# Performance work log

Measured on AMD Instinct MI355X. Metric: run time of the kernel, lower is better.

Reference implementation:

```python
import jax, jax.numpy as jnp
import numpy as np

N_POI, EMBED, N_EDGES, N_LAYERS, N_HEADS = 50000, 128, 800000, 2, 4
B, L = 512, 64  # sessions, session length (equal-length sections)


def setup_inputs() -> dict:
    key = jax.random.key(0)
    ks = jax.random.split(key, 12)
    d = EMBED
    return {
        "poi_embeds": jax.random.normal(ks[0], (N_POI, d), jnp.float32),
        "dist_edges": jax.random.randint(ks[1], (2, N_EDGES), 0, N_POI),
        "dist_vec": jax.random.uniform(ks[2], (N_EDGES,), jnp.float32),
        "data_poi": jax.random.randint(ks[3], (B,), 0, N_POI),
        "data_x": jax.random.randint(ks[4], (B * L,), 0, N_POI),
        "lin_w": jax.random.normal(ks[5], (N_LAYERS, d, d), jnp.float32) / np.sqrt(d),
        "lin_b": jnp.zeros((N_LAYERS, d), jnp.float32),
        "in_proj_w": jax.random.normal(ks[6], (3 * d, d), jnp.float32) / np.sqrt(d),
        "in_proj_b": jnp.zeros((3 * d,), jnp.float32),
        "out_proj_w": jax.random.normal(ks[7], (d, d), jnp.float32) / np.sqrt(d),
        "out_proj_b": jnp.zeros((d,), jnp.float32),
    }


def reference(poi_embeds, dist_edges, dist_vec, data_poi, data_x,
              lin_w, lin_b, in_proj_w, in_proj_b, out_proj_w, out_proj_b):
    n_poi, d = poi_embeds.shape
    # --- edge augmentation done in GeoGraph.__init__: reversed edges + self loops ---
    loop = jnp.arange(n_poi)
    edges = jnp.concatenate([dist_edges, dist_edges[::-1], jnp.stack([loop, loop])], axis=1)
    dvec = jnp.concatenate([dist_vec, dist_vec, jnp.zeros((n_poi,), dist_vec.dtype)])
    src, dst = edges[0], edges[1]
    # degree of source nodes (torch_geometric.utils.degree on nodes1)
    deg = jnp.zeros((n_poi,), poi_embeds.dtype).at[src].add(1.0)
    w = jax.lax.rsqrt(deg[src] * deg[dst]) * jnp.exp(-dvec ** 2)  # [E]

    enc = poi_embeds
    for i in range(lin_w.shape[0]):
        h = enc @ lin_w[i].T + lin_b[i]                              # [N, d]
        msg = w[:, None] * h[dst]                                    # [E, d] gather
        agg = jax.ops.segment_sum(msg, src, num_segments=n_poi)      # [N, d] scatter
        agg = jnp.where(agg >= 0, agg, 0.01 * agg)                   # leaky_relu(0.01)
        enc = agg / jnp.maximum(jnp.linalg.norm(agg, axis=-1, keepdims=True), 1e-12)

    tar_embed = enc[data_poi]                                        # [B, d]
    seq = enc[data_x].reshape(B, L, d)                               # padded sessions

    # --- nn.MultiheadAttention (batch_first) ---
    hd = d // N_HEADS
    qkv = seq @ in_proj_w.T + in_proj_b                              # [B, L, 3d]
    q, k, v = jnp.split(qkv, 3, axis=-1)
    heads = lambda t: t.reshape(B, L, N_HEADS, hd).transpose(0, 2, 1, 3)
    q, k, v = heads(q), heads(k), heads(v)
    scores = jnp.einsum('bhqd,bhkd->bhqk', q, k) / np.sqrt(hd)
    attn = jax.nn.softmax(scores, axis=-1)
    o = jnp.einsum('bhqk,bhkd->bhqd', attn, v).transpose(0, 2, 1, 3).reshape(B, L, d)
    o = o @ out_proj_w.T + out_proj_b

    aggr_feat = o.mean(axis=1)                                       # mean over padded length
    return aggr_feat, tar_embed
```

## Files before the change

### kernel.cpp

```cpp
#include <hip/hip_runtime.h>
#include <hip/hip_fp16.h>

#define NPOI 50000
#define EMB 128
#define NEDGE 800000
#define EAUG (2 * NEDGE + NPOI)
#define BATCH 512
#define SEQL 64
#define NHEADS 4
#define HDIM 32
#define NB 196
#define P1_BLOCKS ((NEDGE + 2047) / 2048)
#define SLAB_CAP 10240
#define BUCKET_CAP 10240

typedef _Float16 half8 __attribute__((ext_vector_type(8)));
typedef _Float16 half4 __attribute__((ext_vector_type(4)));
typedef _Float16 half2t __attribute__((ext_vector_type(2)));
typedef float f32x4 __attribute__((ext_vector_type(4)));
typedef unsigned long long u64;

union HBits { _Float16 h; unsigned short u; };


#define N4_POI (NPOI * 128 / 4)
#define N4_LIN (2 * 128 * 128 / 4)
#define N4_INW (384 * 128 / 4)
#define CVT_TOT (N4_POI + N4_LIN + N4_INW + NB)

__global__ void cvt_all_kernel(const float* __restrict__ poi, const float* __restrict__ linw,
                               const float* __restrict__ inw,
                               _Float16* __restrict__ poi_h, _Float16* __restrict__ linw_h,
                               _Float16* __restrict__ inw_h, int* __restrict__ bcur) {
    int i = blockIdx.x * blockDim.x + threadIdx.x;
    const float* src; _Float16* dst; int j = i;
    if (i < N4_POI) { src = poi; dst = poi_h; }
    else if (i < N4_POI + N4_LIN) { j = i - N4_POI; src = linw; dst = linw_h; }
    else if (i < N4_POI + N4_LIN + N4_INW) { j = i - N4_POI - N4_LIN; src = inw; dst = inw_h; }
    else if (i < CVT_TOT) { int b = i - (N4_POI + N4_LIN + N4_INW); bcur[b] = b * SLAB_CAP; return; }
    else return;
    float4 v = ((const float4*)src)[j];
    half4 h = { (_Float16)v.x, (_Float16)v.y, (_Float16)v.z, (_Float16)v.w };
    ((half4*)dst)[j] = h;
}


__global__ __launch_bounds__(256) void partition_kernel(
    const int* __restrict__ e0, const int* __restrict__ e1,
    const float* __restrict__ dv, int* __restrict__ bcur,
    u64* __restrict__ staging)
{
    __shared__ u64 stg[4096];
    __shared__ int lh[NB], lbase[NB], gb[NB];
    __shared__ int sc[256];
    const int t = threadIdx.x;
    const int blockBase = blockIdx.x * 2048;
    for (int j = t; j < NB; j += 256) lh[j] = 0;
    __syncthreads();

    u64 vals[16];
    unsigned br[16];
#pragma unroll
    for (int i = 0; i < 8; ++i) {
        br[2 * i] = 0xFFFFFFFFu;
        br[2 * i + 1] = 0xFFFFFFFFu;
        int g = blockBase + i * 256 + t;
        if (g < NEDGE) {
            int s = e0[g], d = e1[g];
            unsigned db = __float_as_uint(dv[g]);
            vals[2 * i]     = ((u64)s << 48) | ((u64)d << 32) | db;
            vals[2 * i + 1] = ((u64)d << 48) | ((u64)s << 32) | db;
            int bs = s >> 8, bd = d >> 8;
            int rs = atomicAdd(&lh[bs], 1);
            int rd_ = atomicAdd(&lh[bd], 1);
            br[2 * i]     = ((unsigned)bs << 16) | (unsigned)rs;
            br[2 * i + 1] = ((unsigned)bd << 16) | (unsigned)rd_;
        }
    }
    __syncthreads();
    sc[t] = (t < NB) ? lh[t] : 0;
    __syncthreads();
    for (int o = 1; o < 256; o <<= 1) {
        int u = (t >= o) ? sc[t - o] : 0;
        __syncthreads();
        sc[t] += u;
        __syncthreads();
    }
    if (t < NB) {
        lbase[t] = sc[t] - lh[t];
        gb[t] = (lh[t] > 0) ? atomicAdd(&bcur[t], lh[t]) : 0;
    }
    __syncthreads();
#pragma unroll
    for (int i = 0; i < 16; ++i) {
        if (br[i] != 0xFFFFFFFFu) {
            int b = br[i] >> 16, r = br[i] & 0xFFFF;
            stg[lbase[b] + r] = vals[i];
        }
    }
    __syncthreads();
    const int total = sc[255];
    for (int j = t; j < total; j += 256) {
        u64 v = stg[j];
        int b = (int)(v >> 56);
        staging[(size_t)gb[b] + (unsigned)(j - lbase[b])] = v;
    }
}


__global__ __launch_bounds__(256) void csr_sort_kernel(
    const u64* __restrict__ staging, const int* __restrict__ bcur,
    float* __restrict__ rd, int* __restrict__ offs, unsigned* __restrict__ ew)
{
    const int k = blockIdx.x;
    const int node0 = k * 256;
    __shared__ unsigned outb[BUCKET_CAP];
    __shared__ int cnt[256], base2[256];
    __shared__ float rdl[256];
    __shared__ int bb_sh;
    const int t = threadIdx.x;
    const int node = node0 + t;
    {
        int partial = 0;
        for (int j = t; j < k; j += 256) partial += (bcur[j] - j * SLAB_CAP) + 256;
        base2[t] = partial;
        __syncthreads();
        for (int o = 128; o > 0; o >>= 1) {
            if (t < o) base2[t] += base2[t + o];
            __syncthreads();
        }
        if (t == 0) bb_sh = base2[0];
        __syncthreads();
    }
    const int bucketbase = bb_sh;
    __syncthreads();
    cnt[t] = 0;
    __syncthreads();
    const int sb = k * SLAB_CAP;
    const int n = bcur[k] - sb;
    for (int j = t; j < n; j += 256)
        atomicAdd(&cnt[(int)(staging[sb + j] >> 48) & 255], 1);
    __syncthreads();
    int rowsz = (node < NPOI) ? cnt[t] + 1 : 0;
    if (node < NPOI) {
        float r_ = rsqrtf((float)rowsz);
        rd[node] = r_;
        rdl[t] = r_;
    } else rdl[t] = 0.f;
    base2[t] = rowsz;
    __syncthreads();
    for (int o = 1; o < 256; o <<= 1) {
        int u = (t >= o) ? base2[t - o] : 0;
        __syncthreads();
        base2[t] += u;
        __syncthreads();
    }
    int myexc = base2[t] - rowsz;
    __syncthreads();
    base2[t] = myexc;
    cnt[t] = 0;
    if (node < NPOI) {
        offs[node] = bucketbase + myexc;
        if (node == NPOI - 1) offs[NPOI] = bucketbase + myexc + rowsz;
    }
    __syncthreads();
    for (int j = t; j < n; j += 256) {
        u64 e = staging[sb + j];
        int sl = (int)(e >> 48) & 255;
        int d = (int)(e >> 32) & 0xFFFF;
        float dist = __uint_as_float((unsigned)e);
        float w = rdl[sl] * expf(-dist * dist);
        HBits cv; cv.h = (_Float16)w;
        int r = atomicAdd(&cnt[sl], 1);
        outb[base2[sl] + r] = ((unsigned)d << 16) | cv.u;
    }
    __syncthreads();
    if (node < NPOI) {
        HBits cv; cv.h = (_Float16)rdl[t];
        outb[base2[t] + cnt[t]] = ((unsigned)node << 16) | cv.u;
    }
    __syncthreads();
    const int ntot = n + ((node0 + 256 <= NPOI) ? 256 : (NPOI - node0));
    for (int j = t; j < ntot; j += 256) ew[bucketbase + j] = outb[j];
}


__global__ __launch_bounds__(256) void gemm_mfma_f16(
    const _Float16* __restrict__ A, const int* __restrict__ gidx,
    const _Float16* __restrict__ B, const float* __restrict__ bias,
    const float* __restrict__ rs,
    _Float16* __restrict__ C, int M, int N)
{
    __shared__ _Float16 Asl[64][136];
    __shared__ _Float16 Bsl[64][136];
    const int tid = threadIdx.x;
    const int n0 = blockIdx.x * 64;
    const int m0 = blockIdx.y * 64;

#pragma unroll
    for (int i = 0; i < 4; ++i) {
        int u = i * 256 + tid;
        int r = u >> 4;
        int c = u & 15;
        int row = m0 + r;
        int ar = (row < M) ? (gidx ? gidx[row] : row) : 0;
        *(float4*)&Asl[r][c * 8] = *(const float4*)(A + (size_t)ar * 128 + c * 8);
        *(float4*)&Bsl[r][c * 8] = *(const float4*)(B + (size_t)(n0 + r) * 128 + c * 8);
    }
    __syncthreads();

    const int wave = tid >> 6;
    const int lane = tid & 63;
    const int l15 = lane & 15;
    const int quad = lane >> 4;

    f32x4 acc[4];
#pragma unroll
    for (int mt = 0; mt < 4; ++mt) acc[mt] = (f32x4){0.f, 0.f, 0.f, 0.f};

#pragma unroll
    for (int ks = 0; ks < 4; ++ks) {
        half8 bfrag = *(const half8*)&Bsl[wave * 16 + l15][quad * 8 + ks * 32];
#pragma unroll
        for (int mt = 0; mt < 4; ++mt) {
            half8 afrag = *(const half8*)&Asl[mt * 16 + l15][quad * 8 + ks * 32];
            acc[mt] = __builtin_amdgcn_mfma_f32_16x16x32_f16(afrag, bfrag, acc[mt], 0, 0, 0);
        }
    }

    const int col = wave * 16 + l15;
    const float bv = bias[n0 + col];
    __syncthreads();
#pragma unroll
    for (int mt = 0; mt < 4; ++mt)
#pragma unroll
        for (int r = 0; r < 4; ++r) {
            int m = m0 + mt * 16 + quad * 4 + r;
            float v = acc[mt][r] + bv;
            if (rs) { int mm = (m < M) ? m : 0; v *= rs[mm]; }
            Asl[mt * 16 + quad * 4 + r][col] = (_Float16)v;
        }
    __syncthreads();
#pragma unroll
    for (int i = 0; i < 2; ++i) {
        int u = i * 256 + tid;
        int r = u >> 3;
        int c = u & 7;
        int m = m0 + r;
        if (m < M)
            *(half8*)(C + (size_t)m * N + n0 + c * 8) = *(const half8*)&Asl[r][c * 8];
    }
}


__global__ __launch_bounds__(64) void aggregate_kernel(
    const _Float16* __restrict__ h, const int* __restrict__ offs,
    const unsigned* __restrict__ ew, _Float16* __restrict__ enc_h)
{
    const int row = blockIdx.x;
    const int lane = threadIdx.x;
    const int beg = offs[row];
    const int end = offs[row + 1];
    float ax = 0.f, ay = 0.f;
#pragma unroll 8
    for (int e = beg; e < end; ++e) {
        unsigned p = ew[e];
        HBits cv; cv.u = (unsigned short)(p & 0xffffu);
        float w = (float)cv.h;
        int d = p >> 16;
        half2t hv = *(const half2t*)(h + (size_t)d * 128 + lane * 2);
        ax += w * (float)hv[0];
        ay += w * (float)hv[1];
    }
    ax = ax >= 0.f ? ax : 0.01f * ax;
    ay = ay >= 0.f ? ay : 0.01f * ay;
    float ss = ax * ax + ay * ay;
#pragma unroll
    for (int o = 32; o > 0; o >>= 1) ss += __shfl_xor(ss, o);
    float inv = 1.f / fmaxf(sqrtf(ss), 1e-12f);
    half2t hv = { (_Float16)(ax * inv), (_Float16)(ay * inv) };
    *(half2t*)(enc_h + (size_t)row * 128 + lane * 2) = hv;
}


__global__ __launch_bounds__(256) void attn_mfma_kernel(
    const _Float16* __restrict__ qkv, const float* __restrict__ outw,
    const float* __restrict__ outb, const _Float16* __restrict__ enc_h,
    const int* __restrict__ data_poi, float* __restrict__ out)
{
    const int b = blockIdx.x;
    const int wave = threadIdx.x >> 6;
    const int lane = threadIdx.x & 63;
    const int l15 = lane & 15;
    const int quad = lane >> 4;
    __shared__ _Float16 pP[NHEADS][64][72];
    __shared__ _Float16 vT[NHEADS][32][72];
    __shared__ float ob[128];
    const _Float16* base = qkv + (size_t)b * SEQL * 384;

    {
        const _Float16* vrow = base + (size_t)lane * 384 + 256 + wave * 32;
        half8 v0 = *(const half8*)(vrow);
        half8 v1 = *(const half8*)(vrow + 8);
        half8 v2 = *(const half8*)(vrow + 16);
        half8 v3 = *(const half8*)(vrow + 24);
#pragma unroll
        for (int j = 0; j < 8; ++j) {
            vT[wave][j][lane]      = v0[j];
            vT[wave][j + 8][lane]  = v1[j];
            vT[wave][j + 16][lane] = v2[j];
            vT[wave][j + 24][lane] = v3[j];
        }
    }

    half8 qf[4], kf[4];
#pragma unroll
    for (int t = 0; t < 4; ++t) {
        qf[t] = *(const half8*)(base + (size_t)(t * 16 + l15) * 384 + wave * 32 + quad * 8);
        kf[t] = *(const half8*)(base + (size_t)(t * 16 + l15) * 384 + 128 + wave * 32 + quad * 8);
    }

    f32x4 S[4][4];
#pragma unroll
    for (int lt = 0; lt < 4; ++lt)
#pragma unroll
        for (int mt = 0; mt < 4; ++mt) S[lt][mt] = (f32x4){0.f, 0.f, 0.f, 0.f};
#pragma unroll
    for (int lt = 0; lt < 4; ++lt)
#pragma unroll
        for (int mt = 0; mt < 4; ++mt)
            S[lt][mt] = __builtin_amdgcn_mfma_f32_16x16x32_f16(qf[lt], kf[mt], S[lt][mt], 0, 0, 0);

    const float scale = 0.17677669529663687f;
#pragma unroll
    for (int lt = 0; lt < 4; ++lt) {
#pragma unroll
        for (int r = 0; r < 4; ++r) {
            float m0 = -1e30f;
#pragma unroll
            for (int mt = 0; mt < 4; ++mt) {
                S[lt][mt][r] *= scale;
                m0 = fmaxf(m0, S[lt][mt][r]);
            }
#pragma unroll
            for (int o = 1; o < 16; o <<= 1) m0 = fmaxf(m0, __shfl_xor(m0, o));
            float s0 = 0.f;
#pragma unroll
            for (int mt = 0; mt < 4; ++mt) {
                float p = __expf(S[lt][mt][r] - m0);
                S[lt][mt][r] = p;
                s0 += p;
            }
#pragma unroll
            for (int o = 1; o < 16; o <<= 1) s0 += __shfl_xor(s0, o);
            float inv = 1.f / s0;
#pragma unroll
            for (int mt = 0; mt < 4; ++mt)
                pP[wave][lt * 16 + quad * 4 + r][mt * 16 + l15] = (_Float16)(S[lt][mt][r] * inv);
        }
    }
    __syncthreads();

    f32x4 O[4][2];
#pragma unroll
    for (int lt = 0; lt < 4; ++lt)
#pragma unroll
        for (int jt = 0; jt < 2; ++jt) O[lt][jt] = (f32x4){0.f, 0.f, 0.f, 0.f};
#pragma unroll
    for (int kh = 0; kh < 2; ++kh) {
        half8 vf[2];
#pragma unroll
        for (int jt = 0; jt < 2; ++jt)
            vf[jt] = *(const half8*)&vT[wave][jt * 16 + l15][kh * 32 + quad * 8];
#pragma unroll
        for (int lt = 0; lt < 4; ++lt) {
            half8 pf = *(const half8*)&pP[wave][lt * 16 + l15][kh * 32 + quad * 8];
#pragma unroll
            for (int jt = 0; jt < 2; ++jt)
                O[lt][jt] = __builtin_amdgcn_mfma_f32_16x16x32_f16(pf, vf[jt], O[lt][jt], 0, 0, 0);
        }
    }

#pragma unroll
    for (int jt = 0; jt < 2; ++jt) {
        float part = 0.f;
#pragma unroll
        for (int lt = 0; lt < 4; ++lt)
#pragma unroll
            for (int r = 0; r < 4; ++r) part += O[lt][jt][r];
        part += __shfl_xor(part, 16);
        part += __shfl_xor(part, 32);
        if (quad == 0) ob[wave * 32 + jt * 16 + l15] = part * (1.f / 64.f);
    }
    __syncthreads();

    int t = threadIdx.x;
    if (t < 128) {
        float val = outb[t];
        const float* wrow = outw + (size_t)t * 128;
#pragma unroll 8
        for (int k4 = 0; k4 < 32; ++k4) {
            float4 wv = *(const float4*)(wrow + k4 * 4);
            val += wv.x * ob[k4 * 4] + wv.y * ob[k4 * 4 + 1]
                 + wv.z * ob[k4 * 4 + 2] + wv.w * ob[k4 * 4 + 3];
        }
        out[(size_t)b * 128 + t] = val;
    } else {
        int j = t - 128;
        out[(size_t)(BATCH + b) * 128 + j] = (float)enc_h[(size_t)data_poi[b] * 128 + j];
    }
}


extern "C" void kernel_launch(void* const* d_in, const int* in_sizes, int n_in,
                              void* d_out, int out_size, void* d_ws, size_t ws_size,
                              hipStream_t stream)
{
    const float* poi      = (const float*)d_in[0];
    const int*   edges    = (const int*)d_in[1];
    const float* dvec     = (const float*)d_in[2];
    const int*   data_poi = (const int*)d_in[3];
    const int*   data_x   = (const int*)d_in[4];
    const float* lin_w    = (const float*)d_in[5];
    const float* lin_b    = (const float*)d_in[6];
    const float* inw      = (const float*)d_in[7];
    const float* inb      = (const float*)d_in[8];
    const float* outw     = (const float*)d_in[9];
    const float* outb     = (const float*)d_in[10];
    const int* e0 = edges;
    const int* e1 = edges + NEDGE;

    char* ws = (char*)d_ws;
    size_t off = 0;
    auto alloc = [&](size_t bytes) -> void* {
        void* p = ws + off;
        off = (off + bytes + 255) & ~(size_t)255;
        return p;
    };
    int*      offs   = (int*)     alloc((NPOI + 1) * 4);
    int*      bcur   = (int*)     alloc(NB * 4);
    float*    rd     = (float*)   alloc(NPOI * 4);
    unsigned* ew     = (unsigned*)alloc((size_t)EAUG * 4);
    _Float16* enc_h  = (_Float16*)alloc((size_t)NPOI * 128 * 2);
    _Float16* linw_h = (_Float16*)alloc((size_t)2 * 128 * 128 * 2);
    _Float16* inw_h  = (_Float16*)alloc((size_t)384 * 128 * 2);
    char*     big    = (char*)    alloc(50ull * 1024 * 1024);
    _Float16* poi_h   = (_Float16*)big;
    u64*      staging = (u64*)(big + 16ull * 1024 * 1024);
    _Float16* hbuf    = (_Float16*)(big + 33ull * 1024 * 1024);
    _Float16* qkv_h   = (_Float16*)big;

    cvt_all_kernel<<<(CVT_TOT + 255) / 256, 256, 0, stream>>>(
        poi, lin_w, inw, poi_h, linw_h, inw_h, bcur);

    partition_kernel<<<P1_BLOCKS, 256, 0, stream>>>(e0, e1, dvec, bcur, staging);
    csr_sort_kernel<<<NB, 256, 0, stream>>>(staging, bcur, rd, offs, ew);

    gemm_mfma_f16<<<dim3(2, (NPOI + 63) / 64), 256, 0, stream>>>(
        poi_h, nullptr, linw_h, lin_b, rd, hbuf, NPOI, 128);
    aggregate_kernel<<<NPOI, 64, 0, stream>>>(hbuf, offs, ew, enc_h);
    gemm_mfma_f16<<<dim3(2, (NPOI + 63) / 64), 256, 0, stream>>>(
        enc_h, nullptr, linw_h + 128 * 128, lin_b + 128, rd, hbuf, NPOI, 128);
    aggregate_kernel<<<NPOI, 64, 0, stream>>>(hbuf, offs, ew, enc_h);

    gemm_mfma_f16<<<dim3(6, BATCH * SEQL / 64), 256, 0, stream>>>(
        enc_h, data_x, inw_h, inb, nullptr, qkv_h, BATCH * SEQL, 384);
    attn_mfma_kernel<<<BATCH, 256, 0, stream>>>(qkv_h, outw, outb, enc_h, data_poi,
                                                (float*)d_out);
}
```

Before: 282.7 us.

## Fuse fp32-to-fp16 POI conversion into GEMM and double GEMM row tile

Removes the separate conversion pass over the 50000x128 POI embedding table: the first layer GEMM now reads fp32 rows directly and converts them to half while staging into shared memory. The GEMM is templated on the A element type, and its M tile grows from 64 to 128 rows, so each block reuses the B tile over twice as many rows with 8 accumulators per wave. This saves one full write and read of the half-precision POI copy, at the cost of more shared memory and registers per block and half as many blocks.

```diff
diff --git a/kernel.cpp b/kernel.cpp
--- a/kernel.cpp
+++ b/kernel.cpp
@@ -1,5 +1,6 @@
 #include <hip/hip_runtime.h>
 #include <hip/hip_fp16.h>
+#include <type_traits>
 
 #define NPOI 50000
 #define EMB 128
@@ -23,21 +24,18 @@
 union HBits { _Float16 h; unsigned short u; };
 
 
-#define N4_POI (NPOI * 128 / 4)
 #define N4_LIN (2 * 128 * 128 / 4)
 #define N4_INW (384 * 128 / 4)
-#define CVT_TOT (N4_POI + N4_LIN + N4_INW + NB)
-
-__global__ void cvt_all_kernel(const float* __restrict__ poi, const float* __restrict__ linw,
-                               const float* __restrict__ inw,
-                               _Float16* __restrict__ poi_h, _Float16* __restrict__ linw_h,
-                               _Float16* __restrict__ inw_h, int* __restrict__ bcur) {
+#define CVT_TOT (N4_LIN + N4_INW + NB)
+
+__global__ void cvt_all_kernel(const float* __restrict__ linw, const float* __restrict__ inw,
+                               _Float16* __restrict__ linw_h, _Float16* __restrict__ inw_h,
+                               int* __restrict__ bcur) {
     int i = blockIdx.x * blockDim.x + threadIdx.x;
     const float* src; _Float16* dst; int j = i;
-    if (i < N4_POI) { src = poi; dst = poi_h; }
-    else if (i < N4_POI + N4_LIN) { j = i - N4_POI; src = linw; dst = linw_h; }
-    else if (i < N4_POI + N4_LIN + N4_INW) { j = i - N4_POI - N4_LIN; src = inw; dst = inw_h; }
-    else if (i < CVT_TOT) { int b = i - (N4_POI + N4_LIN + N4_INW); bcur[b] = b * SLAB_CAP; return; }
+    if (i < N4_LIN) { src = linw; dst = linw_h; }
+    else if (i < N4_LIN + N4_INW) { j = i - N4_LIN; src = inw; dst = inw_h; }
+    else if (i < CVT_TOT) { int b = i - (N4_LIN + N4_INW); bcur[b] = b * SLAB_CAP; return; }
     else return;
     float4 v = ((const float4*)src)[j];
     half4 h = { (_Float16)v.x, (_Float16)v.y, (_Float16)v.z, (_Float16)v.w };
@@ -185,26 +183,44 @@
 }
 
 
+template <typename AT>
 __global__ __launch_bounds__(256) void gemm_mfma_f16(
-    const _Float16* __restrict__ A, const int* __restrict__ gidx,
+    const AT* __restrict__ A, const int* __restrict__ gidx,
     const _Float16* __restrict__ B, const float* __restrict__ bias,
     const float* __restrict__ rs,
     _Float16* __restrict__ C, int M, int N)
 {
-    __shared__ _Float16 Asl[64][136];
+    __shared__ _Float16 Asl[128][136];
     __shared__ _Float16 Bsl[64][136];
     const int tid = threadIdx.x;
     const int n0 = blockIdx.x * 64;
-    const int m0 = blockIdx.y * 64;
-
+    const int m0 = blockIdx.y * 128;
+
+    if constexpr (std::is_same<AT, _Float16>::value) {
+#pragma unroll
+        for (int i = 0; i < 8; ++i) {
+            int u = i * 256 + tid;
+            int r = u >> 4, c = u & 15;
+            int row = m0 + r;
+            int ar = (row < M) ? (gidx ? gidx[row] : row) : 0;
+            *(float4*)&Asl[r][c * 8] = *(const float4*)(A + (size_t)ar * 128 + c * 8);
+        }
+    } else {
+#pragma unroll
+        for (int i = 0; i < 16; ++i) {
+            int u = i * 256 + tid;
+            int r = u >> 5, c = u & 31;
+            int row = m0 + r;
+            int ar = (row < M) ? (gidx ? gidx[row] : row) : 0;
+            float4 v = *(const float4*)(A + (size_t)ar * 128 + c * 4);
+            half4 h = { (_Float16)v.x, (_Float16)v.y, (_Float16)v.z, (_Float16)v.w };
+            *(half4*)&Asl[r][c * 4] = h;
+        }
+    }
 #pragma unroll
     for (int i = 0; i < 4; ++i) {
         int u = i * 256 + tid;
-        int r = u >> 4;
-        int c = u & 15;
-        int row = m0 + r;
-        int ar = (row < M) ? (gidx ? gidx[row] : row) : 0;
-        *(float4*)&Asl[r][c * 8] = *(const float4*)(A + (size_t)ar * 128 + c * 8);
+        int r = u >> 4, c = u & 15;
         *(float4*)&Bsl[r][c * 8] = *(const float4*)(B + (size_t)(n0 + r) * 128 + c * 8);
     }
     __syncthreads();
@@ -214,15 +230,15 @@
     const int l15 = lane & 15;
     const int quad = lane >> 4;
 
-    f32x4 acc[4];
-#pragma unroll
-    for (int mt = 0; mt < 4; ++mt) acc[mt] = (f32x4){0.f, 0.f, 0.f, 0.f};
+    f32x4 acc[8];
+#pragma unroll
+    for (int mt = 0; mt < 8; ++mt) acc[mt] = (f32x4){0.f, 0.f, 0.f, 0.f};
 
 #pragma unroll
     for (int ks = 0; ks < 4; ++ks) {
         half8 bfrag = *(const half8*)&Bsl[wave * 16 + l15][quad * 8 + ks * 32];
 #pragma unroll
-        for (int mt = 0; mt < 4; ++mt) {
+        for (int mt = 0; mt < 8; ++mt) {
             half8 afrag = *(const half8*)&Asl[mt * 16 + l15][quad * 8 + ks * 32];
             acc[mt] = __builtin_amdgcn_mfma_f32_16x16x32_f16(afrag, bfrag, acc[mt], 0, 0, 0);
         }
@@ -232,7 +248,7 @@
     const float bv = bias[n0 + col];
     __syncthreads();
 #pragma unroll
-    for (int mt = 0; mt < 4; ++mt)
+    for (int mt = 0; mt < 8; ++mt)
 #pragma unroll
         for (int r = 0; r < 4; ++r) {
             int m = m0 + mt * 16 + quad * 4 + r;
@@ -242,7 +258,7 @@
         }
     __syncthreads();
 #pragma unroll
-    for (int i = 0; i < 2; ++i) {
+    for (int i = 0; i < 4; ++i) {
         int u = i * 256 + tid;
         int r = u >> 3;
         int c = u & 7;
@@ -445,25 +461,24 @@
     _Float16* linw_h = (_Float16*)alloc((size_t)2 * 128 * 128 * 2);
     _Float16* inw_h  = (_Float16*)alloc((size_t)384 * 128 * 2);
     char*     big    = (char*)    alloc(50ull * 1024 * 1024);
-    _Float16* poi_h   = (_Float16*)big;
     u64*      staging = (u64*)(big + 16ull * 1024 * 1024);
     _Float16* hbuf    = (_Float16*)(big + 33ull * 1024 * 1024);
     _Float16* qkv_h   = (_Float16*)big;
 
     cvt_all_kernel<<<(CVT_TOT + 255) / 256, 256, 0, stream>>>(
-        poi, lin_w, inw, poi_h, linw_h, inw_h, bcur);
+        lin_w, inw, linw_h, inw_h, bcur);
 
     partition_kernel<<<P1_BLOCKS, 256, 0, stream>>>(e0, e1, dvec, bcur, staging);
     csr_sort_kernel<<<NB, 256, 0, stream>>>(staging, bcur, rd, offs, ew);
 
-    gemm_mfma_f16<<<dim3(2, (NPOI + 63) / 64), 256, 0, stream>>>(
-        poi_h, nullptr, linw_h, lin_b, rd, hbuf, NPOI, 128);
+    gemm_mfma_f16<float><<<dim3(2, (NPOI + 127) / 128), 256, 0, stream>>>(
+        poi, nullptr, linw_h, lin_b, rd, hbuf, NPOI, 128);
     aggregate_kernel<<<NPOI, 64, 0, stream>>>(hbuf, offs, ew, enc_h);
-    gemm_mfma_f16<<<dim3(2, (NPOI + 63) / 64), 256, 0, stream>>>(
+    gemm_mfma_f16<_Float16><<<dim3(2, (NPOI + 127) / 128), 256, 0, stream>>>(
         enc_h, nullptr, linw_h + 128 * 128, lin_b + 128, rd, hbuf, NPOI, 128);
     aggregate_kernel<<<NPOI, 64, 0, stream>>>(hbuf, offs, ew, enc_h);
 
-    gemm_mfma_f16<<<dim3(6, BATCH * SEQL / 64), 256, 0, stream>>>(
+    gemm_mfma_f16<_Float16><<<dim3(6, BATCH * SEQL / 128), 256, 0, stream>>>(
         enc_h, data_x, inw_h, inb, nullptr, qkv_h, BATCH * SEQL, 384);
     attn_mfma_kernel<<<BATCH, 256, 0, stream>>>(qkv_h, outw, outb, enc_h, data_poi,
                                                 (float*)d_out);
```

Measured after the change: 292.8 us. 3.6% more time.

## Fuse edge partition, first-layer GEMM and weight conversion into one launch

Applied to the files above, without the earlier changes.

Drops the separate fp32-to-fp16 conversion of the full POI embedding table. The first linear layer now converts fp32 inputs to fp16 directly while loading shared-memory tiles. That GEMM runs as extra blocks of the same launch as the edge partition and the weight conversion, so independent work can share the GPU. The per-row rsqrt(degree) scaling that the first GEMM used to apply is moved to the end of csr_sort, which rescales the GEMM output rows in place once degrees are known. Bucket counters are now zeroed with a memset and stored as relative offsets. This removes a full pass over the embedding table and two launches, at the cost of an extra read-modify-write of hbuf in csr_sort.

```diff
diff --git a/kernel.cpp b/kernel.cpp
--- a/kernel.cpp
+++ b/kernel.cpp
@@ -8,11 +8,18 @@
 #define BATCH 512
 #define SEQL 64
 #define NHEADS 4
-#define HDIM 32
 #define NB 196
 #define P1_BLOCKS ((NEDGE + 2047) / 2048)
 #define SLAB_CAP 10240
 #define BUCKET_CAP 10240
+
+#define N4_LIN (2 * 128 * 128 / 4)
+#define N4_INW (384 * 128 / 4)
+#define CVTW_TOT (N4_LIN + N4_INW)
+#define CVTW_BLOCKS ((CVTW_TOT + 255) / 256)
+#define GB1_Y ((NPOI + 63) / 64)
+#define GB1 (2 * GB1_Y)
+#define FUSED_BLOCKS (P1_BLOCKS + GB1 + CVTW_BLOCKS)
 
 typedef _Float16 half8 __attribute__((ext_vector_type(8)));
 typedef _Float16 half4 __attribute__((ext_vector_type(4)));
@@ -22,40 +29,27 @@
 
 union HBits { _Float16 h; unsigned short u; };
 
-
-#define N4_POI (NPOI * 128 / 4)
-#define N4_LIN (2 * 128 * 128 / 4)
-#define N4_INW (384 * 128 / 4)
-#define CVT_TOT (N4_POI + N4_LIN + N4_INW + NB)
-
-__global__ void cvt_all_kernel(const float* __restrict__ poi, const float* __restrict__ linw,
-                               const float* __restrict__ inw,
-                               _Float16* __restrict__ poi_h, _Float16* __restrict__ linw_h,
-                               _Float16* __restrict__ inw_h, int* __restrict__ bcur) {
-    int i = blockIdx.x * blockDim.x + threadIdx.x;
-    const float* src; _Float16* dst; int j = i;
-    if (i < N4_POI) { src = poi; dst = poi_h; }
-    else if (i < N4_POI + N4_LIN) { j = i - N4_POI; src = linw; dst = linw_h; }
-    else if (i < N4_POI + N4_LIN + N4_INW) { j = i - N4_POI - N4_LIN; src = inw; dst = inw_h; }
-    else if (i < CVT_TOT) { int b = i - (N4_POI + N4_LIN + N4_INW); bcur[b] = b * SLAB_CAP; return; }
-    else return;
-    float4 v = ((const float4*)src)[j];
-    half4 h = { (_Float16)v.x, (_Float16)v.y, (_Float16)v.z, (_Float16)v.w };
-    ((half4*)dst)[j] = h;
-}
-
-
-__global__ __launch_bounds__(256) void partition_kernel(
-    const int* __restrict__ e0, const int* __restrict__ e1,
-    const float* __restrict__ dv, int* __restrict__ bcur,
-    u64* __restrict__ staging)
-{
-    __shared__ u64 stg[4096];
-    __shared__ int lh[NB], lbase[NB], gb[NB];
-    __shared__ int sc[256];
+struct __align__(16) SmemP {
+    u64 stg[4096];
+    int lh[NB], lbase[NB], gb[NB];
+    int sc[256];
+};
+struct __align__(16) SmemG {
+    _Float16 Asl[64][136];
+    _Float16 Bsl[64][136];
+};
+#define SMEM_BYTES (sizeof(SmemP) > sizeof(SmemG) ? sizeof(SmemP) : sizeof(SmemG))
+
+
+__device__ void partition_body(char* smem_raw, int bb,
+                               const int* __restrict__ e0, const int* __restrict__ e1,
+                               const float* __restrict__ dv, int* __restrict__ bcur,
+                               u64* __restrict__ staging)
+{
+    SmemP& S = *(SmemP*)smem_raw;
     const int t = threadIdx.x;
-    const int blockBase = blockIdx.x * 2048;
-    for (int j = t; j < NB; j += 256) lh[j] = 0;
+    const int blockBase = bb * 2048;
+    for (int j = t; j < NB; j += 256) S.lh[j] = 0;
     __syncthreads();
 
     u64 vals[16];
@@ -71,46 +65,139 @@
             vals[2 * i]     = ((u64)s << 48) | ((u64)d << 32) | db;
             vals[2 * i + 1] = ((u64)d << 48) | ((u64)s << 32) | db;
             int bs = s >> 8, bd = d >> 8;
-            int rs = atomicAdd(&lh[bs], 1);
-            int rd_ = atomicAdd(&lh[bd], 1);
+            int rs = atomicAdd(&S.lh[bs], 1);
+            int rd_ = atomicAdd(&S.lh[bd], 1);
             br[2 * i]     = ((unsigned)bs << 16) | (unsigned)rs;
             br[2 * i + 1] = ((unsigned)bd << 16) | (unsigned)rd_;
         }
     }
     __syncthreads();
-    sc[t] = (t < NB) ? lh[t] : 0;
+    S.sc[t] = (t < NB) ? S.lh[t] : 0;
     __syncthreads();
     for (int o = 1; o < 256; o <<= 1) {
-        int u = (t >= o) ? sc[t - o] : 0;
+        int u = (t >= o) ? S.sc[t - o] : 0;
         __syncthreads();
-        sc[t] += u;
+        S.sc[t] += u;
         __syncthreads();
     }
     if (t < NB) {
-        lbase[t] = sc[t] - lh[t];
-        gb[t] = (lh[t] > 0) ? atomicAdd(&bcur[t], lh[t]) : 0;
+        S.lbase[t] = S.sc[t] - S.lh[t];
+        S.gb[t] = (S.lh[t] > 0) ? (t * SLAB_CAP + atomicAdd(&bcur[t], S.lh[t])) : 0;
     }
     __syncthreads();
 #pragma unroll
     for (int i = 0; i < 16; ++i) {
         if (br[i] != 0xFFFFFFFFu) {
             int b = br[i] >> 16, r = br[i] & 0xFFFF;
-            stg[lbase[b] + r] = vals[i];
-        }
-    }
-    __syncthreads();
-    const int total = sc[255];
+            S.stg[S.lbase[b] + r] = vals[i];
+        }
+    }
+    __syncthreads();
+    const int total = S.sc[255];
     for (int j = t; j < total; j += 256) {
-        u64 v = stg[j];
+        u64 v = S.stg[j];
         int b = (int)(v >> 56);
-        staging[(size_t)gb[b] + (unsigned)(j - lbase[b])] = v;
-    }
+        staging[(size_t)S.gb[b] + (unsigned)(j - S.lbase[b])] = v;
+    }
+}
+
+__device__ void gemm1_body(char* smem_raw, int g, const float* __restrict__ A,
+                           const float* __restrict__ B, const float* __restrict__ bias,
+                           _Float16* __restrict__ C)
+{
+    SmemG& S = *(SmemG*)smem_raw;
+    const int tid = threadIdx.x;
+    const int n0 = (g / GB1_Y) * 64;
+    const int m0 = (g % GB1_Y) * 64;
+
+#pragma unroll
+    for (int i = 0; i < 8; ++i) {
+        int u = i * 256 + tid;
+        int r = u >> 5, c = u & 31;
+        int row = m0 + r;
+        int ar = (row < NPOI) ? row : 0;
+        float4 v = *(const float4*)(A + (size_t)ar * 128 + c * 4);
+        half4 h = { (_Float16)v.x, (_Float16)v.y, (_Float16)v.z, (_Float16)v.w };
+        *(half4*)&S.Asl[r][c * 4] = h;
+        float4 bv = *(const float4*)(B + (size_t)(n0 + r) * 128 + c * 4);
+        half4 hb = { (_Float16)bv.x, (_Float16)bv.y, (_Float16)bv.z, (_Float16)bv.w };
+        *(half4*)&S.Bsl[r][c * 4] = hb;
+    }
+    __syncthreads();
+
+    const int wave = tid >> 6;
+    const int lane = tid & 63;
+    const int l15 = lane & 15;
+    const int quad = lane >> 4;
+
+    f32x4 acc[4];
+#pragma unroll
+    for (int mt = 0; mt < 4; ++mt) acc[mt] = (f32x4){0.f, 0.f, 0.f, 0.f};
+#pragma unroll
+    for (int ks = 0; ks < 4; ++ks) {
+        half8 bfrag = *(const half8*)&S.Bsl[wave * 16 + l15][quad * 8 + ks * 32];
+#pragma unroll
+        for (int mt = 0; mt < 4; ++mt) {
+            half8 afrag = *(const half8*)&S.Asl[mt * 16 + l15][quad * 8 + ks * 32];
+            acc[mt] = __builtin_amdgcn_mfma_f32_16x16x32_f16(afrag, bfrag, acc[mt], 0, 0, 0);
+        }
+    }
+
+    const int col = wave * 16 + l15;
+    const float bv = bias[n0 + col];
+    __syncthreads();
+#pragma unroll
+    for (int mt = 0; mt < 4; ++mt)
+#pragma unroll
+        for (int r = 0; r < 4; ++r)
+            S.Asl[mt * 16 + quad * 4 + r][col] = (_Float16)(acc[mt][r] + bv);
+    __syncthreads();
+#pragma unroll
+    for (int i = 0; i < 2; ++i) {
+        int u = i * 256 + tid;
+        int r = u >> 3, c = u & 7;
+        int m = m0 + r;
+        if (m < NPOI)
+            *(half8*)(C + (size_t)m * 128 + n0 + c * 8) = *(const half8*)&S.Asl[r][c * 8];
+    }
+}
+
+__device__ void cvtw_body(int g, const float* __restrict__ linw, const float* __restrict__ inw,
+                          _Float16* __restrict__ linw_h, _Float16* __restrict__ inw_h)
+{
+    int i = g * 256 + threadIdx.x;
+    if (i >= CVTW_TOT) return;
+    const float* src; _Float16* dst; int j = i;
+    if (i < N4_LIN) { src = linw; dst = linw_h; }
+    else { j = i - N4_LIN; src = inw; dst = inw_h; }
+    float4 v = ((const float4*)src)[j];
+    half4 h = { (_Float16)v.x, (_Float16)v.y, (_Float16)v.z, (_Float16)v.w };
+    ((half4*)dst)[j] = h;
+}
+
+__global__ __launch_bounds__(256) void fused1_kernel(
+    const int* __restrict__ e0, const int* __restrict__ e1, const float* __restrict__ dv,
+    int* __restrict__ bcur, u64* __restrict__ staging,
+    const float* __restrict__ poi, const float* __restrict__ linw,
+    const float* __restrict__ lin_b, _Float16* __restrict__ hbuf,
+    const float* __restrict__ inw, _Float16* __restrict__ linw_h,
+    _Float16* __restrict__ inw_h)
+{
+    __shared__ __align__(16) char smem_raw[SMEM_BYTES];
+    int bx = blockIdx.x;
+    if (bx < P1_BLOCKS)
+        partition_body(smem_raw, bx, e0, e1, dv, bcur, staging);
+    else if (bx < P1_BLOCKS + GB1)
+        gemm1_body(smem_raw, bx - P1_BLOCKS, poi, linw, lin_b, hbuf);
+    else
+        cvtw_body(bx - P1_BLOCKS - GB1, linw, inw, linw_h, inw_h);
 }
 
 
 __global__ __launch_bounds__(256) void csr_sort_kernel(
     const u64* __restrict__ staging, const int* __restrict__ bcur,
-    float* __restrict__ rd, int* __restrict__ offs, unsigned* __restrict__ ew)
+    float* __restrict__ rd, int* __restrict__ offs, unsigned* __restrict__ ew,
+    _Float16* __restrict__ hbuf)
 {
     const int k = blockIdx.x;
     const int node0 = k * 256;
@@ -122,7 +209,7 @@
     const int node = node0 + t;
     {
         int partial = 0;
-        for (int j = t; j < k; j += 256) partial += (bcur[j] - j * SLAB_CAP) + 256;
+        for (int j = t; j < k; j += 256) partial += bcur[j] + 256;
         base2[t] = partial;
         __syncthreads();
         for (int o = 128; o > 0; o >>= 1) {
@@ -137,7 +224,7 @@
     cnt[t] = 0;
     __syncthreads();
     const int sb = k * SLAB_CAP;
-    const int n = bcur[k] - sb;
+    const int n = bcur[k];
     for (int j = t; j < n; j += 256)
         atomicAdd(&cnt[(int)(staging[sb + j] >> 48) & 255], 1);
     __syncthreads();
@@ -180,8 +267,18 @@
         outb[base2[t] + cnt[t]] = ((unsigned)node << 16) | cv.u;
     }
     __syncthreads();
-    const int ntot = n + ((node0 + 256 <= NPOI) ? 256 : (NPOI - node0));
+    const int nn = (node0 + 256 <= NPOI) ? 256 : (NPOI - node0);
+    const int ntot = n + nn;
     for (int j = t; j < ntot; j += 256) ew[bucketbase + j] = outb[j];
+    __syncthreads();
+    for (int rr = (t >> 4); rr < nn; rr += 16) {
+        float s = rdl[rr];
+        half8* p = (half8*)(hbuf + (size_t)(node0 + rr) * 128 + (t & 15) * 8);
+        half8 v = *p;
+#pragma unroll
+        for (int j = 0; j < 8; ++j) v[j] = (_Float16)((float)v[j] * s);
+        *p = v;
+    }
 }
 
 
@@ -445,19 +542,17 @@
     _Float16* linw_h = (_Float16*)alloc((size_t)2 * 128 * 128 * 2);
     _Float16* inw_h  = (_Float16*)alloc((size_t)384 * 128 * 2);
     char*     big    = (char*)    alloc(50ull * 1024 * 1024);
-    _Float16* poi_h   = (_Float16*)big;
     u64*      staging = (u64*)(big + 16ull * 1024 * 1024);
     _Float16* hbuf    = (_Float16*)(big + 33ull * 1024 * 1024);
     _Float16* qkv_h   = (_Float16*)big;
 
-    cvt_all_kernel<<<(CVT_TOT + 255) / 256, 256, 0, stream>>>(
-        poi, lin_w, inw, poi_h, linw_h, inw_h, bcur);
-
-    partition_kernel<<<P1_BLOCKS, 256, 0, stream>>>(e0, e1, dvec, bcur, staging);
-    csr_sort_kernel<<<NB, 256, 0, stream>>>(staging, bcur, rd, offs, ew);
-
-    gemm_mfma_f16<<<dim3(2, (NPOI + 63) / 64), 256, 0, stream>>>(
-        poi_h, nullptr, linw_h, lin_b, rd, hbuf, NPOI, 128);
+    hipMemsetAsync(bcur, 0, NB * 4, stream);
+
+    fused1_kernel<<<FUSED_BLOCKS, 256, 0, stream>>>(
+        e0, e1, dvec, bcur, staging, poi, lin_w, lin_b, hbuf, inw, linw_h, inw_h);
+
+    csr_sort_kernel<<<NB, 256, 0, stream>>>(staging, bcur, rd, offs, ew, hbuf);
+
     aggregate_kernel<<<NPOI, 64, 0, stream>>>(hbuf, offs, ew, enc_h);
     gemm_mfma_f16<<<dim3(2, (NPOI + 63) / 64), 256, 0, stream>>>(
         enc_h, nullptr, linw_h + 128 * 128, lin_b + 128, rd, hbuf, NPOI, 128);
```

After: 270.5 us. 1.05x faster.
